# Kernel tuning notes

Hardware: AMD Instinct MI355X
Metric: run time of the kernel (lower is better)

## Reference

```python
import jax, jax.numpy as jnp
import numpy as np

B = 16           # batch graphs
C = 2            # canonical orderings
STEPS = 64       # subgraphs (generation steps) per ordering
NUM_SUB = B * C * STEPS          # 2048 segments
EDGES_PER_SUB = 1024
E = NUM_SUB * EDGES_PER_SUB      # 2,097,152 augmented edges
K = 20                           # mixture components
POS_WEIGHT = 1.0                 # BCEWithLogitsLoss pos_weight (edge_weight)


def setup_inputs() -> dict:
    key = jax.random.key(0)
    k1, k2, k3 = jax.random.split(key, 3)
    label = jax.random.bernoulli(k1, 0.3, (E,)).astype(jnp.float32)
    log_theta = jax.random.normal(k2, (E, K), dtype=jnp.float32)
    log_alpha = jax.random.normal(k3, (E, K), dtype=jnp.float32)
    subgraph_idx = jnp.repeat(jnp.arange(NUM_SUB, dtype=jnp.int32), EDGES_PER_SUB)
    # cumulative subgraph counts per batch graph (C*STEPS subgraphs each)
    subgraph_idx_base = jnp.arange(B + 1, dtype=jnp.int32) * (C * STEPS)
    return {
        "label": label,
        "log_theta": log_theta,
        "log_alpha": log_alpha,
        "subgraph_idx": subgraph_idx,
        "subgraph_idx_base": subgraph_idx_base,
        "num_canonical_order": C,
        "num_subgraph": NUM_SUB,
    }


def _bce_with_logits(x, y):
    # torch BCEWithLogitsLoss(pos_weight=w, reduction='none')
    return POS_WEIGHT * y * jax.nn.softplus(-x) + (1.0 - y) * jax.nn.softplus(x)


def _mixture_bernoulli_loss(label, log_theta, log_alpha, subgraph_idx,
                            subgraph_idx_base, C, num_subgraph):
    nB = subgraph_idx_base.shape[0] - 1
    seg = subgraph_idx.astype(jnp.int32)

    # per-edge, per-component BCE nll: [E, K]
    adj_nll = _bce_with_logits(log_theta, label[:, None])
    # mask out last edge of each subgraph segment
    mask = jnp.concatenate([seg[:-1] == seg[1:], jnp.array([False])])
    adj_nll = adj_nll * mask[:, None].astype(adj_nll.dtype)

    ones_e = jnp.ones_like(label)
    num_edges_per_subgraph = jax.ops.segment_sum(ones_e, seg, num_segments=num_subgraph)
    reduce_adj_nll = jax.ops.segment_sum(adj_nll, seg, num_segments=num_subgraph)
    reduce_log_alpha = jax.ops.segment_sum(log_alpha, seg, num_segments=num_subgraph)
    reduce_log_alpha = reduce_log_alpha / num_edges_per_subgraph[:, None]
    reduce_log_alpha = jax.nn.log_softmax(reduce_log_alpha, axis=-1)

    # mixture log-likelihood per subgraph: [num_subgraph]
    log_prob = jax.scipy.special.logsumexp(-reduce_adj_nll + reduce_log_alpha, axis=1)

    # map each subgraph -> (graph, ordering) bucket index in [0, B*C)
    s = jnp.arange(num_subgraph, dtype=jnp.int32)
    b = jnp.searchsorted(subgraph_idx_base, s, side="right").astype(jnp.int32) - 1
    per_batch = subgraph_idx_base[b + 1] - subgraph_idx_base[b]
    bc_size = per_batch // C
    bc_idx = b * C + (s - subgraph_idx_base[b]) // bc_size

    bc_log_prob = jax.ops.segment_sum(log_prob, bc_idx, num_segments=nB * C)
    bc_const = jax.ops.segment_sum(num_edges_per_subgraph, bc_idx, num_segments=nB * C)
    bc_loss = (bc_log_prob / bc_const).reshape(nB, C)
    bc_log_prob = bc_log_prob.reshape(nB, C)

    b_log_prob = jax.scipy.special.logsumexp(bc_log_prob, axis=1)
    b_loss = jax.scipy.special.logsumexp(bc_loss, axis=1)

    b_loss = -b_loss
    rewards = jnp.ones(nB, dtype=b_loss.dtype)  # rewards=None path, baseline=0
    pos_loss = b_loss * rewards * (rewards > 0).astype(b_loss.dtype)
    neg_loss = jnp.log(1.0 - jnp.exp(-b_loss) + 1e-6) * rewards * (rewards < 0).astype(b_loss.dtype)
    loss = neg_loss + pos_loss
    return loss.mean()  # reduction='mean'


def reference(label, log_theta, log_alpha, subgraph_idx, subgraph_idx_base,
              num_canonical_order, num_subgraph):
    return _mixture_bernoulli_loss(label, log_theta, log_alpha, subgraph_idx,
                                   subgraph_idx_base, num_canonical_order,
                                   num_subgraph)
```

## Files before the change

kernel.cpp:

```cpp
#include <hip/hip_runtime.h>
#include <math.h>

#define KC 20
#define EPS 1024
#define NUM_SUB 2048
#define NBUCKET 32
#define SUBS_PER_BUCKET 64
#define NB 16
#define NBLK1 4096
#define HALF 512

typedef float f4 __attribute__((ext_vector_type(4)));

__global__ __launch_bounds__(320, 6) void gran_pass1a(
    const float* __restrict__ label,
    const float* __restrict__ log_theta,
    const float* __restrict__ log_alpha,
    float* __restrict__ pT,
    float* __restrict__ pA)
{
    const int h = blockIdx.x;
    const int t = threadIdx.x;
    const int q = t / 5;

    const long base_e  = (long)h * HALF;
    const long base_p4 = (long)h * (HALF * KC / 4) + t;

    const f4* __restrict__ th4 = (const f4*)log_theta;
    const f4* __restrict__ al4 = (const f4*)log_alpha;

    float y[8];
#pragma unroll
    for (int m = 0; m < 8; ++m)
        y[m] = __builtin_nontemporal_load(&label[base_e + q + 64 * m]);

    float accT[4] = {0.f, 0.f, 0.f, 0.f};
    float accA[4] = {0.f, 0.f, 0.f, 0.f};

#pragma unroll
    for (int mb = 0; mb < 8; mb += 4) {
        f4 th[4], al[4];
#pragma unroll
        for (int u = 0; u < 4; ++u) {
            th[u] = __builtin_nontemporal_load(&th4[base_p4 + 320 * (mb + u)]);
            al[u] = __builtin_nontemporal_load(&al4[base_p4 + 320 * (mb + u)]);
        }
#pragma unroll
        for (int u = 0; u < 4; ++u) {
            const int   m   = mb + u;
            const int   le  = q + 64 * m;
            const float msk = (((h & 1) == 1) && (le == HALF - 1)) ? 0.f : 1.f;
            const float yy  = y[m];
            const float xs[4] = {th[u][0], th[u][1], th[u][2], th[u][3]};
            const float av[4] = {al[u][0], al[u][1], al[u][2], al[u][3]};
#pragma unroll
            for (int c = 0; c < 4; ++c) {
                const float x = xs[c];
                const float sp  = __logf(1.0f + __expf(-fabsf(x)));
                const float bce = fmaxf(x, 0.f) - yy * x + sp;
                accT[c] += msk * bce;
                accA[c] += av[c];
            }
        }
    }

    __shared__ float sT[320 * 4];
    __shared__ float sA[320 * 4];
#pragma unroll
    for (int c = 0; c < 4; ++c) { sT[t * 4 + c] = accT[c]; sA[t * 4 + c] = accA[c]; }
    __syncthreads();

    __shared__ float mT[16 * KC];
    __shared__ float mA[16 * KC];
    {
        float st = 0.f, sa = 0.f;
#pragma unroll
        for (int i = 0; i < 4; ++i) { st += sT[t + 320 * i]; sa += sA[t + 320 * i]; }
        mT[t] = st;
        mA[t] = sa;
    }
    __syncthreads();

    if (t < KC) {
        float st = 0.f, sa = 0.f;
#pragma unroll
        for (int g = 0; g < 16; ++g) { st += mT[g * KC + t]; sa += mA[g * KC + t]; }
        pT[(long)h * KC + t] = st;
        pA[(long)h * KC + t] = sa;
    }
}

__global__ __launch_bounds__(256) void gran_pass1b(
    const float* __restrict__ pT,
    const float* __restrict__ pA,
    float* __restrict__ log_prob_out)
{
    const int s = blockIdx.x * 256 + threadIdx.x;
    if (s >= NUM_SUB) return;
    const long b0 = (long)(2 * s) * KC;
    const long b1 = (long)(2 * s + 1) * KC;

    float vT[KC], vA[KC];
#pragma unroll
    for (int k = 0; k < KC; ++k) {
        vT[k] = pT[b0 + k] + pT[b1 + k];
        vA[k] = (pA[b0 + k] + pA[b1 + k]) * (1.0f / EPS);
    }
    float mx = vA[0];
#pragma unroll
    for (int k = 1; k < KC; ++k) mx = fmaxf(mx, vA[k]);
    float sum = 0.f;
#pragma unroll
    for (int k = 0; k < KC; ++k) sum += expf(vA[k] - mx);
    const float lse = mx + logf(sum);
    float M = -3.4e38f;
    float v[KC];
#pragma unroll
    for (int k = 0; k < KC; ++k) { v[k] = vA[k] - lse - vT[k]; M = fmaxf(M, v[k]); }
    float s2 = 0.f;
#pragma unroll
    for (int k = 0; k < KC; ++k) s2 += expf(v[k] - M);
    log_prob_out[s] = M + logf(s2);
}

__global__ __launch_bounds__(256) void gran_pass2(
    const float* __restrict__ log_prob, float* __restrict__ out)
{
    const int t = threadIdx.x;
    const int bucket = t >> 3;
    const int r      = t & 7;
    double s = 0.0;
    const float* p = log_prob + (long)bucket * SUBS_PER_BUCKET + r * 8;
#pragma unroll
    for (int i = 0; i < 8; ++i) s += (double)p[i];

    __shared__ double part[256];
    part[t] = s;
    __syncthreads();

    __shared__ double bc_loss[NBUCKET];
    if (t < NBUCKET) {
        double b = 0.0;
#pragma unroll
        for (int rr = 0; rr < 8; ++rr) b += part[t * 8 + rr];
        bc_loss[t] = b / (double)(SUBS_PER_BUCKET * EPS);
    }
    __syncthreads();
    if (t == 0) {
        double total = 0.0;
        for (int b = 0; b < NB; ++b) {
            const double a = bc_loss[2 * b];
            const double c = bc_loss[2 * b + 1];
            const double m = fmax(a, c);
            const double lsv = m + log(exp(a - m) + exp(c - m));
            total += -lsv;
        }
        out[0] = (float)(total / (double)NB);
    }
}

extern "C" void kernel_launch(void* const* d_in, const int* in_sizes, int n_in,
                              void* d_out, int out_size, void* d_ws, size_t ws_size,
                              hipStream_t stream) {
    const float* label     = (const float*)d_in[0];
    const float* log_theta = (const float*)d_in[1];
    const float* log_alpha = (const float*)d_in[2];

    float* pT       = (float*)d_ws;
    float* pA       = pT + (long)NBLK1 * KC;
    float* log_prob = pA + (long)NBLK1 * KC;
    float* out      = (float*)d_out;

    gran_pass1a<<<NBLK1, 320, 0, stream>>>(label, log_theta, log_alpha, pT, pA);
    gran_pass1b<<<(NUM_SUB + 255) / 256, 256, 0, stream>>>(pT, pA, log_prob);
    gran_pass2<<<1, 256, 0, stream>>>(log_prob, out);
}
```

Baseline: 328.1 us.

## Fuse per-subgraph reduction and log-softmax into one block per subgraph

The kernel now has one block per subgraph (2048 blocks) instead of two half-subgraph blocks. Each block finishes the component reduction and the log-softmax/logsumexp itself, which removes the intermediate pT/pA partial buffers and the separate pass1b launch. Label loads move inside the loop, which is unrolled by 2. Each block does twice the work, so there are half as many blocks to hide memory latency, and a single thread runs the serial epilogue.

Measured after the change: 358.6 us. 9.3% more time.

```diff
diff --git a/kernel.cpp b/kernel.cpp
--- a/kernel.cpp
+++ b/kernel.cpp
@@ -7,39 +7,35 @@
 #define NBUCKET 32
 #define SUBS_PER_BUCKET 64
 #define NB 16
-#define NBLK1 4096
-#define HALF 512
 
 typedef float f4 __attribute__((ext_vector_type(4)));
 
-__global__ __launch_bounds__(320, 6) void gran_pass1a(
+__global__ __launch_bounds__(320, 6) void gran_pass1(
     const float* __restrict__ label,
     const float* __restrict__ log_theta,
     const float* __restrict__ log_alpha,
-    float* __restrict__ pT,
-    float* __restrict__ pA)
+    float* __restrict__ log_prob_out)
 {
-    const int h = blockIdx.x;
+    const int s = blockIdx.x;
     const int t = threadIdx.x;
     const int q = t / 5;
 
-    const long base_e  = (long)h * HALF;
-    const long base_p4 = (long)h * (HALF * KC / 4) + t;
+    const long base_e  = (long)s * EPS;
+    const long base_p4 = (long)s * (EPS * KC / 4) + t;
 
     const f4* __restrict__ th4 = (const f4*)log_theta;
     const f4* __restrict__ al4 = (const f4*)log_alpha;
 
-    float y[8];
-#pragma unroll
-    for (int m = 0; m < 8; ++m)
-        y[m] = __builtin_nontemporal_load(&label[base_e + q + 64 * m]);
-
     float accT[4] = {0.f, 0.f, 0.f, 0.f};
     float accA[4] = {0.f, 0.f, 0.f, 0.f};
 
+#pragma unroll 2
+    for (int mb = 0; mb < 16; mb += 4) {
+        float y[4];
+        f4 th[4], al[4];
 #pragma unroll
-    for (int mb = 0; mb < 8; mb += 4) {
-        f4 th[4], al[4];
+        for (int u = 0; u < 4; ++u)
+            y[u] = __builtin_nontemporal_load(&label[base_e + q + 64 * (mb + u)]);
 #pragma unroll
         for (int u = 0; u < 4; ++u) {
             th[u] = __builtin_nontemporal_load(&th4[base_p4 + 320 * (mb + u)]);
@@ -47,10 +43,9 @@
         }
 #pragma unroll
         for (int u = 0; u < 4; ++u) {
-            const int   m   = mb + u;
-            const int   le  = q + 64 * m;
-            const float msk = (((h & 1) == 1) && (le == HALF - 1)) ? 0.f : 1.f;
-            const float yy  = y[m];
+            const int   le  = q + 64 * (mb + u);
+            const float msk = (le == EPS - 1) ? 0.f : 1.f;
+            const float yy  = y[u];
             const float xs[4] = {th[u][0], th[u][1], th[u][2], th[u][3]};
             const float av[4] = {al[u][0], al[u][1], al[u][2], al[u][3]};
 #pragma unroll
@@ -81,46 +76,35 @@
     }
     __syncthreads();
 
+    __shared__ float rT[KC];
+    __shared__ float rA[KC];
     if (t < KC) {
         float st = 0.f, sa = 0.f;
 #pragma unroll
         for (int g = 0; g < 16; ++g) { st += mT[g * KC + t]; sa += mA[g * KC + t]; }
-        pT[(long)h * KC + t] = st;
-        pA[(long)h * KC + t] = sa;
+        rT[t] = st;
+        rA[t] = sa * (1.0f / EPS);
     }
-}
+    __syncthreads();
 
-__global__ __launch_bounds__(256) void gran_pass1b(
-    const float* __restrict__ pT,
-    const float* __restrict__ pA,
-    float* __restrict__ log_prob_out)
-{
-    const int s = blockIdx.x * 256 + threadIdx.x;
-    if (s >= NUM_SUB) return;
-    const long b0 = (long)(2 * s) * KC;
-    const long b1 = (long)(2 * s + 1) * KC;
+    if (t == 0) {
+        float mx = rA[0];
+#pragma unroll
+        for (int k = 1; k < KC; ++k) mx = fmaxf(mx, rA[k]);
+        float sum = 0.f;
+#pragma unroll
+        for (int k = 0; k < KC; ++k) sum += expf(rA[k] - mx);
+        const float lse = mx + logf(sum);
 
-    float vT[KC], vA[KC];
+        float M = -3.4e38f;
+        float v[KC];
 #pragma unroll
-    for (int k = 0; k < KC; ++k) {
-        vT[k] = pT[b0 + k] + pT[b1 + k];
-        vA[k] = (pA[b0 + k] + pA[b1 + k]) * (1.0f / EPS);
+        for (int k = 0; k < KC; ++k) { v[k] = rA[k] - lse - rT[k]; M = fmaxf(M, v[k]); }
+        float s2 = 0.f;
+#pragma unroll
+        for (int k = 0; k < KC; ++k) s2 += expf(v[k] - M);
+        log_prob_out[s] = M + logf(s2);
     }
-    float mx = vA[0];
-#pragma unroll
-    for (int k = 1; k < KC; ++k) mx = fmaxf(mx, vA[k]);
-    float sum = 0.f;
-#pragma unroll
-    for (int k = 0; k < KC; ++k) sum += expf(vA[k] - mx);
-    const float lse = mx + logf(sum);
-    float M = -3.4e38f;
-    float v[KC];
-#pragma unroll
-    for (int k = 0; k < KC; ++k) { v[k] = vA[k] - lse - vT[k]; M = fmaxf(M, v[k]); }
-    float s2 = 0.f;
-#pragma unroll
-    for (int k = 0; k < KC; ++k) s2 += expf(v[k] - M);
-    log_prob_out[s] = M + logf(s2);
 }
 
 __global__ __launch_bounds__(256) void gran_pass2(
@@ -166,12 +150,9 @@
     const float* log_theta = (const float*)d_in[1];
     const float* log_alpha = (const float*)d_in[2];
 
-    float* pT       = (float*)d_ws;
-    float* pA       = pT + (long)NBLK1 * KC;
-    float* log_prob = pA + (long)NBLK1 * KC;
+    float* log_prob = (float*)d_ws;
     float* out      = (float*)d_out;
 
-    gran_pass1a<<<NBLK1, 320, 0, stream>>>(label, log_theta, log_alpha, pT, pA);
-    gran_pass1b<<<(NUM_SUB + 255) / 256, 256, 0, stream>>>(pT, pA, log_prob);
+    gran_pass1<<<NUM_SUB, 320, 0, stream>>>(label, log_theta, log_alpha, log_prob);
     gran_pass2<<<1, 256, 0, stream>>>(log_prob, out);
 }
```
